# Performance work log

Hardware: AMD Instinct MI355X
Metric: run time of the kernel (lower is better)

## Reference

```python
import jax, jax.numpy as jnp
import numpy as np

NUM_CLASSES = 10
HIDDEN = 64
_LABEL2MASK_THRESHOL = 500


def setup_inputs() -> dict:
    key = jax.random.key(0)
    ks = jax.random.split(key, 8)
    B, h, w = 4, 60, 80
    feature1 = jax.random.normal(ks[0], (B, 512, h, w), dtype=jnp.float32)
    feature2 = jax.random.normal(ks[1], (B, 512, h // 2, w // 2), dtype=jnp.float32)
    # kaiming fan_in init for 1x1 convs: std = sqrt(2/fan_in)
    w1 = jax.random.normal(ks[2], (HIDDEN, 512), dtype=jnp.float32) * np.sqrt(2.0 / 512)
    b1 = jnp.zeros((HIDDEN,), dtype=jnp.float32)
    w2 = jax.random.normal(ks[3], (HIDDEN, 512), dtype=jnp.float32) * np.sqrt(2.0 / 512)
    b2 = jnp.zeros((HIDDEN,), dtype=jnp.float32)
    wo = jax.random.normal(ks[4], (NUM_CLASSES + 1, HIDDEN), dtype=jnp.float32) * np.sqrt(2.0 / HIDDEN)
    bo = jnp.zeros((NUM_CLASSES + 1,), dtype=jnp.float32)
    return {"feature1": feature1, "feature2": feature2, "w1": w1, "b1": b1,
            "w2": w2, "b2": b2, "wo": wo, "bo": bo}


def conv1x1(x, w, b):
    # x: (B,C,H,W), w: (O,C) -> (B,O,H,W)
    return jnp.einsum('bchw,oc->bohw', x, w) + b[None, :, None, None]


def label2bbx(seg, num_classes):
    # seg: (B,H,W) int labels. Vectorized per-(batch,class) min/max reduction
    # replacing the original python double loop. Fixed output shape
    # (B*(num_classes-1), 6); rows failing the pixel-count threshold are -1.
    B, H, W = seg.shape
    classes = jnp.arange(1, num_classes)  # cls_id != 0, covers 1..num_classes-1
    mask = seg[:, None, :, :] == classes[None, :, None, None]  # (B,C-1,H,W)
    count = mask.sum(axis=(2, 3))
    xs = jnp.arange(W)
    ys = jnp.arange(H)
    big = jnp.int32(2 ** 30)
    xmin = jnp.where(mask, xs[None, None, None, :], big).min(axis=(2, 3))
    xmax = jnp.where(mask, xs[None, None, None, :], -1).max(axis=(2, 3))
    ymin = jnp.where(mask, ys[None, None, :, None], big).min(axis=(2, 3))
    ymax = jnp.where(mask, ys[None, None, :, None], -1).max(axis=(2, 3))
    valid = count >= _LABEL2MASK_THRESHOL
    batch_ids = jnp.broadcast_to(jnp.arange(B)[:, None], (B, num_classes - 1))
    cls_ids = jnp.broadcast_to(classes[None, :], (B, num_classes - 1))
    rows = jnp.stack([batch_ids, xmin, ymin, xmax, ymax, cls_ids], axis=-1)
    rows = jnp.where(valid[..., None], rows, -1)
    return rows.reshape(-1, 6)


def reference(feature1, feature2, w1, b1, w2, b2, wo, bo):
    feat1 = jax.nn.relu(conv1x1(feature1, w1, b1))          # (B,64,h,w)
    feat2 = jax.nn.relu(conv1x1(feature2, w2, b2))          # (B,64,h/2,w/2)
    feat2_up = jnp.repeat(jnp.repeat(feat2, 2, axis=2), 2, axis=3)
    combo = feat1 + feat2_up
    # nearest upsample scale_factor=8
    combo_up = jnp.repeat(jnp.repeat(combo, 8, axis=2), 8, axis=3)  # (B,64,8h,8w)
    out = jax.nn.relu(conv1x1(combo_up, wo, bo))            # (B,11,8h,8w)
    probability = jax.nn.softmax(out, axis=1)
    segmentation = jnp.argmax(probability, axis=1)
    bbx = label2bbx(segmentation, NUM_CLASSES)
    return probability, segmentation, bbx
```

## Files before the change

kernel.cpp:

```cpp
#include <hip/hip_runtime.h>
#include <math.h>

#define NB   4
#define CIN  512
#define HID  64
#define NK   11
#define H1   60
#define W1p  80
#define P1   4800
#define H2   30
#define W2p  40
#define P2   1200
#define HO   480
#define WOp  640
#define NP1  (NB*P1)
#define NP2  (NB*P2)
#define PLANE ((size_t)HO*WOp)
#define SEG_OFF ((size_t)NB*NK*PLANE)
#define BBX_OFF (SEG_OFF + (size_t)NB*PLANE)

#define WS_WT1 0
#define WS_WT2 32768
#define WS_C1  65536
#define WS_F2  (WS_C1 + NP1*64)
#define WS_PRB (WS_F2 + NP2*64)
#define WS_SEG (WS_PRB + NP1*12)

__global__ __launch_bounds__(256) void transpose_w(const float* __restrict__ w1,
                                                   const float* __restrict__ w2,
                                                   float* __restrict__ ws) {
    int i = blockIdx.x * 256 + threadIdx.x;
    if (i >= HID * CIN) return;
    int o = i >> 9;
    int c = i & 511;
    ws[WS_WT1 + c * HID + o] = w1[i];
    ws[WS_WT2 + c * HID + o] = w2[i];
}

__global__ __launch_bounds__(256) void conv_krg(const float* __restrict__ f1,
                                                const float* __restrict__ f2,
                                                const float* __restrict__ wt1,
                                                const float* __restrict__ wt2,
                                                const float* __restrict__ b1v,
                                                const float* __restrict__ b2v,
                                                float* __restrict__ c1o,
                                                float* __restrict__ f2o) {
    __shared__ float red[3][16][256];
    int D = blockIdx.x;
    int L = (D & 7) * 48 + (D >> 3);
    int tile = L >> 2;
    int rg   = L & 3;
    const float* X; const float* wT; const float* bias; float* Cout;
    int P, px0;
    if (tile < 76) {
        int b = tile / 19; int ti = tile % 19;
        px0 = ti * 256; if (px0 > P1 - 256) px0 = P1 - 256;
        X = f1 + (size_t)b * CIN * P1;  P = P1;  wT = wt1;  bias = b1v;
        Cout = c1o + (size_t)b * P1 * 64;
    } else {
        int u = tile - 76; int b = u / 5; int ti = u % 5;
        px0 = ti * 256; if (px0 > P2 - 256) px0 = P2 - 256;
        X = f2 + (size_t)b * CIN * P2;  P = P2;  wT = wt2;  bias = b2v;
        Cout = f2o + (size_t)b * P2 * 64;
    }
    int lane  = threadIdx.x & 63;
    int kq    = threadIdx.x >> 6;
    int cbase = __builtin_amdgcn_readfirstlane(kq << 7);
    int row0  = rg << 4;

    const float* Xp = X + (size_t)cbase * P + px0 + lane * 4;
    const float* Wp = wT + (size_t)cbase * 64 + row0;

    float acc[16][4];
#pragma unroll
    for (int r = 0; r < 16; ++r)
#pragma unroll
        for (int q = 0; q < 4; ++q) acc[r][q] = 0.f;

    float4 xa[4], xn[4];
#pragma unroll
    for (int i = 0; i < 4; ++i) xa[i] = *(const float4*)(Xp + (size_t)i * P);

    for (int c0 = 0; c0 < 128; c0 += 4) {
        if (c0 < 124) {
#pragma unroll
            for (int i = 0; i < 4; ++i)
                xn[i] = *(const float4*)(Xp + (size_t)(c0 + 4 + i) * P);
        }
#pragma unroll
        for (int i = 0; i < 4; ++i) {
            const float* wr = Wp + (size_t)(c0 + i) * 64;
            float4 x = xa[i];
#pragma unroll
            for (int r4 = 0; r4 < 4; ++r4) {
                float4 w = *(const float4*)(wr + r4 * 4);
#pragma unroll
                for (int j = 0; j < 4; ++j) {
                    int r = r4 * 4 + j;
                    float wv = (j == 0) ? w.x : (j == 1) ? w.y : (j == 2) ? w.z : w.w;
                    acc[r][0] = fmaf(x.x, wv, acc[r][0]);
                    acc[r][1] = fmaf(x.y, wv, acc[r][1]);
                    acc[r][2] = fmaf(x.z, wv, acc[r][2]);
                    acc[r][3] = fmaf(x.w, wv, acc[r][3]);
                }
            }
        }
#pragma unroll
        for (int i = 0; i < 4; ++i) xa[i] = xn[i];
    }

    if (kq > 0) {
#pragma unroll
        for (int r = 0; r < 16; ++r)
            *(float4*)&red[kq - 1][r][lane * 4] =
                make_float4(acc[r][0], acc[r][1], acc[r][2], acc[r][3]);
    }
    __syncthreads();
    if (kq == 0) {
        float v[16][4];
#pragma unroll
        for (int r = 0; r < 16; ++r) {
            float4 s0 = *(float4*)&red[0][r][lane * 4];
            float4 s1 = *(float4*)&red[1][r][lane * 4];
            float4 s2 = *(float4*)&red[2][r][lane * 4];
            float bb = bias[row0 + r];
            float a0 = acc[r][0] + s0.x + s1.x + s2.x + bb;
            float a1 = acc[r][1] + s0.y + s1.y + s2.y + bb;
            float a2 = acc[r][2] + s0.z + s1.z + s2.z + bb;
            float a3 = acc[r][3] + s0.w + s1.w + s2.w + bb;
            v[r][0] = a0 > 0.f ? a0 : 0.f;
            v[r][1] = a1 > 0.f ? a1 : 0.f;
            v[r][2] = a2 > 0.f ? a2 : 0.f;
            v[r][3] = a3 > 0.f ? a3 : 0.f;
        }
#pragma unroll
        for (int q = 0; q < 4; ++q) {
            float* op = Cout + (size_t)(px0 + lane * 4 + q) * 64 + row0;
#pragma unroll
            for (int r4 = 0; r4 < 4; ++r4)
                *(float4*)(op + r4 * 4) = make_float4(v[r4*4+0][q], v[r4*4+1][q],
                                                      v[r4*4+2][q], v[r4*4+3][q]);
        }
    }
}

__global__ __launch_bounds__(256) void head_kernel(const float* __restrict__ wo,
                                                   const float* __restrict__ bo,
                                                   float* __restrict__ ws) {
    __shared__ float swo[NK * 64];
    __shared__ float sbo[NK];
    for (int i = threadIdx.x; i < NK * 64; i += 256) swo[i] = wo[i];
    if (threadIdx.x < NK) sbo[threadIdx.x] = bo[threadIdx.x];
    __syncthreads();

    int p  = blockIdx.x * 256 + threadIdx.x;
    int b  = p / P1;
    int pb = p % P1;
    int y  = pb / W1p, x = pb % W1p;
    int qp = (y >> 1) * W2p + (x >> 1);
    const float* c1p = ws + WS_C1 + ((size_t)b * P1 + pb) * 64;
    const float* f2p = ws + WS_F2 + ((size_t)b * P2 + qp) * 64;

    float ok[NK];
#pragma unroll
    for (int k = 0; k < NK; ++k) ok[k] = sbo[k];
#pragma unroll
    for (int o4 = 0; o4 < 16; ++o4) {
        float4 c1q = *(const float4*)(c1p + o4 * 4);
        float4 f2q = *(const float4*)(f2p + o4 * 4);
        float co[4] = { c1q.x + f2q.x, c1q.y + f2q.y, c1q.z + f2q.z, c1q.w + f2q.w };
#pragma unroll
        for (int j = 0; j < 4; ++j) {
            int o = o4 * 4 + j;
#pragma unroll
            for (int k = 0; k < NK; ++k) ok[k] = fmaf(co[j], swo[k * 64 + o], ok[k]);
        }
    }
    float m = 0.f;
#pragma unroll
    for (int k = 0; k < NK; ++k) {
        ok[k] = ok[k] > 0.f ? ok[k] : 0.f;
        if (ok[k] > m) m = ok[k];
    }
    float e[NK], sum = 0.f;
#pragma unroll
    for (int k = 0; k < NK; ++k) { e[k] = expf(ok[k] - m); sum += e[k]; }
    float inv = 1.f / sum;
    int arg = 0; float best = ok[0];
#pragma unroll
    for (int k = 1; k < NK; ++k) { if (ok[k] > best) { best = ok[k]; arg = k; } }

    float* pr = ws + WS_PRB + (size_t)p * 12;
#pragma unroll
    for (int k = 0; k < NK; ++k) pr[k] = e[k] * inv;
    pr[11] = (float)arg;
    ((int*)(ws + WS_SEG))[p] = arg;
}

__global__ __launch_bounds__(256) void upsample_kernel(const float* __restrict__ ws,
                                                       float* __restrict__ out) {
    const float* prb = ws + WS_PRB;
    unsigned total4 = (unsigned)((SEG_OFF + (size_t)NB * PLANE) / 4);
    unsigned step = gridDim.x * 256;
    for (unsigned i4 = blockIdx.x * 256 + threadIdx.x; i4 < total4; i4 += step) {
        unsigned f = i4 * 4;
        float v;
        if (f < (unsigned)SEG_OFF) {
            unsigned plane = f / (unsigned)PLANE;
            unsigned r = f - plane * (unsigned)PLANE;
            unsigned b = plane / NK, k = plane - b * NK;
            unsigned y = r / WOp, x = r - y * WOp;
            unsigned p = b * P1 + (y >> 3) * W1p + (x >> 3);
            v = prb[p * 12 + k];
        } else {
            unsigned g = f - (unsigned)SEG_OFF;
            unsigned b = g / (unsigned)PLANE;
            unsigned r = g - b * (unsigned)PLANE;
            unsigned y = r / WOp, x = r - y * WOp;
            unsigned p = b * P1 + (y >> 3) * W1p + (x >> 3);
            v = prb[p * 12 + 11];
        }
        *(float4*)(out + f) = make_float4(v, v, v, v);
    }
}

__global__ __launch_bounds__(256) void bbx_kernel(const float* __restrict__ ws,
                                                  float* __restrict__ out) {
    __shared__ int cnt[10], xmn[10], xmx[10], ymn[10], ymx[10];
    int b = blockIdx.x;
    int t = threadIdx.x;
    if (t < 10) { cnt[t] = 0; xmn[t] = 1 << 30; xmx[t] = -1; ymn[t] = 1 << 30; ymx[t] = -1; }
    __syncthreads();
    const int* seg = (const int*)(ws + WS_SEG) + b * P1;
    for (int p = t; p < P1; p += 256) {
        int s = seg[p];
        if (s >= 1 && s <= 9) {
            int y = p / W1p, x = p % W1p;
            atomicAdd(&cnt[s], 1);
            atomicMin(&xmn[s], x); atomicMax(&xmx[s], x);
            atomicMin(&ymn[s], y); atomicMax(&ymx[s], y);
        }
    }
    __syncthreads();
    if (t < 9) {
        int c = t + 1;
        bool valid = cnt[c] * 64 >= 500;
        float r[6];
        if (valid) {
            r[0] = (float)b;
            r[1] = (float)(xmn[c] * 8);
            r[2] = (float)(ymn[c] * 8);
            r[3] = (float)(xmx[c] * 8 + 7);
            r[4] = (float)(ymx[c] * 8 + 7);
            r[5] = (float)c;
        } else {
            for (int i = 0; i < 6; ++i) r[i] = -1.f;
        }
        float* row = out + BBX_OFF + (size_t)(b * 9 + t) * 6;
        for (int i = 0; i < 6; ++i) row[i] = r[i];
    }
}

extern "C" void kernel_launch(void* const* d_in, const int* in_sizes, int n_in,
                              void* d_out, int out_size, void* d_ws, size_t ws_size,
                              hipStream_t stream) {
    const float* f1 = (const float*)d_in[0];
    const float* f2 = (const float*)d_in[1];
    const float* w1 = (const float*)d_in[2];
    const float* b1 = (const float*)d_in[3];
    const float* w2 = (const float*)d_in[4];
    const float* b2 = (const float*)d_in[5];
    const float* wo = (const float*)d_in[6];
    const float* bo = (const float*)d_in[7];
    float* ws  = (float*)d_ws;
    float* out = (float*)d_out;

    transpose_w<<<128, 256, 0, stream>>>(w1, w2, ws);
    conv_krg<<<384, 256, 0, stream>>>(f1, f2, ws + WS_WT1, ws + WS_WT2,
                                      b1, b2, ws + WS_C1, ws + WS_F2);
    head_kernel<<<75, 256, 0, stream>>>(wo, bo, ws);
    upsample_kernel<<<2048, 256, 0, stream>>>(ws, out);
    bbx_kernel<<<NB, 256, 0, stream>>>(ws, out);
}
```

Measured before the change: 68.34 us.

## Split conv output rows into 8-row groups, stage weights in LDS, deepen prefetch

The 1x1 conv kernel now gives each block 8 output channels instead of 16, which doubles the grid to 768 blocks. Each block stages its weight slice (512x8) in shared memory rather than reading the weights from global memory. Input loads are double-buffered in chunks of 8 channels to hide latency better. The trade is that each input tile is now read from global memory by twice as many blocks, and there is an extra sync and LDS fill per block. In return the kernel gets more parallelism and lower register pressure.

```diff
diff --git a/kernel.cpp b/kernel.cpp
--- a/kernel.cpp
+++ b/kernel.cpp
@@ -37,7 +37,7 @@
     ws[WS_WT2 + c * HID + o] = w2[i];
 }
 
-__global__ __launch_bounds__(256) void conv_krg(const float* __restrict__ f1,
+__global__ __launch_bounds__(256) void conv_v10(const float* __restrict__ f1,
                                                 const float* __restrict__ f2,
                                                 const float* __restrict__ wt1,
                                                 const float* __restrict__ wt2,
@@ -45,11 +45,14 @@
                                                 const float* __restrict__ b2v,
                                                 float* __restrict__ c1o,
                                                 float* __restrict__ f2o) {
-    __shared__ float red[3][16][256];
+    __shared__ float wlds[CIN * 8];
+    __shared__ float red[3][8][256];
     int D = blockIdx.x;
-    int L = (D & 7) * 48 + (D >> 3);
-    int tile = L >> 2;
-    int rg   = L & 3;
+    int L = (D & 7) * 96 + (D >> 3);
+    int tile = L >> 3;
+    int rg   = L & 7;
+    int row0 = rg << 3;
+
     const float* X; const float* wT; const float* bias; float* Cout;
     int P, px0;
     if (tile < 76) {
@@ -63,63 +66,84 @@
         X = f2 + (size_t)b * CIN * P2;  P = P2;  wT = wt2;  bias = b2v;
         Cout = f2o + (size_t)b * P2 * 64;
     }
+
+    {
+        int t = threadIdx.x;
+        int c2 = t >> 1, part = (t & 1) * 4;
+#pragma unroll
+        for (int i = 0; i < 4; ++i) {
+            int c = c2 + i * 128;
+            float4 w = *(const float4*)(wT + (size_t)c * 64 + row0 + part);
+            *(float4*)&wlds[c * 8 + part] = w;
+        }
+    }
+    __syncthreads();
+
     int lane  = threadIdx.x & 63;
     int kq    = threadIdx.x >> 6;
-    int cbase = __builtin_amdgcn_readfirstlane(kq << 7);
-    int row0  = rg << 4;
+    int cbase = kq << 7;
 
     const float* Xp = X + (size_t)cbase * P + px0 + lane * 4;
-    const float* Wp = wT + (size_t)cbase * 64 + row0;
-
-    float acc[16][4];
-#pragma unroll
-    for (int r = 0; r < 16; ++r)
+
+    float acc[8][4];
+#pragma unroll
+    for (int r = 0; r < 8; ++r)
 #pragma unroll
         for (int q = 0; q < 4; ++q) acc[r][q] = 0.f;
 
-    float4 xa[4], xn[4];
-#pragma unroll
-    for (int i = 0; i < 4; ++i) xa[i] = *(const float4*)(Xp + (size_t)i * P);
-
-    for (int c0 = 0; c0 < 128; c0 += 4) {
-        if (c0 < 124) {
-#pragma unroll
-            for (int i = 0; i < 4; ++i)
-                xn[i] = *(const float4*)(Xp + (size_t)(c0 + 4 + i) * P);
-        }
-#pragma unroll
-        for (int i = 0; i < 4; ++i) {
-            const float* wr = Wp + (size_t)(c0 + i) * 64;
-            float4 x = xa[i];
-#pragma unroll
-            for (int r4 = 0; r4 < 4; ++r4) {
-                float4 w = *(const float4*)(wr + r4 * 4);
-#pragma unroll
-                for (int j = 0; j < 4; ++j) {
-                    int r = r4 * 4 + j;
-                    float wv = (j == 0) ? w.x : (j == 1) ? w.y : (j == 2) ? w.z : w.w;
-                    acc[r][0] = fmaf(x.x, wv, acc[r][0]);
-                    acc[r][1] = fmaf(x.y, wv, acc[r][1]);
-                    acc[r][2] = fmaf(x.z, wv, acc[r][2]);
-                    acc[r][3] = fmaf(x.w, wv, acc[r][3]);
-                }
+    float4 xA[8], xB[8];
+
+    auto comp8 = [&](const float4* xb, int cq) {
+#pragma unroll
+        for (int i = 0; i < 8; ++i) {
+            const float* wq = wlds + (size_t)(cbase + cq + i) * 8;
+            float4 w0 = *(const float4*)(wq);
+            float4 w1 = *(const float4*)(wq + 4);
+            float4 x  = xb[i];
+#pragma unroll
+            for (int j = 0; j < 4; ++j) {
+                float wv0 = (j == 0) ? w0.x : (j == 1) ? w0.y : (j == 2) ? w0.z : w0.w;
+                float wv1 = (j == 0) ? w1.x : (j == 1) ? w1.y : (j == 2) ? w1.z : w1.w;
+                acc[j][0]     = fmaf(x.x, wv0, acc[j][0]);
+                acc[j][1]     = fmaf(x.y, wv0, acc[j][1]);
+                acc[j][2]     = fmaf(x.z, wv0, acc[j][2]);
+                acc[j][3]     = fmaf(x.w, wv0, acc[j][3]);
+                acc[j + 4][0] = fmaf(x.x, wv1, acc[j + 4][0]);
+                acc[j + 4][1] = fmaf(x.y, wv1, acc[j + 4][1]);
+                acc[j + 4][2] = fmaf(x.z, wv1, acc[j + 4][2]);
+                acc[j + 4][3] = fmaf(x.w, wv1, acc[j + 4][3]);
             }
         }
-#pragma unroll
-        for (int i = 0; i < 4; ++i) xa[i] = xn[i];
+    };
+
+#pragma unroll
+    for (int i = 0; i < 8; ++i) xA[i] = *(const float4*)(Xp + (size_t)i * P);
+
+    for (int it = 0; it < 8; ++it) {
+        int c0 = it * 16;
+#pragma unroll
+        for (int i = 0; i < 8; ++i)
+            xB[i] = *(const float4*)(Xp + (size_t)(c0 + 8 + i) * P);
+        comp8(xA, c0);
+        if (it < 7) {
+#pragma unroll
+            for (int i = 0; i < 8; ++i)
+                xA[i] = *(const float4*)(Xp + (size_t)(c0 + 16 + i) * P);
+        }
+        comp8(xB, c0 + 8);
     }
 
     if (kq > 0) {
 #pragma unroll
-        for (int r = 0; r < 16; ++r)
+        for (int r = 0; r < 8; ++r)
             *(float4*)&red[kq - 1][r][lane * 4] =
                 make_float4(acc[r][0], acc[r][1], acc[r][2], acc[r][3]);
     }
     __syncthreads();
     if (kq == 0) {
-        float v[16][4];
-#pragma unroll
-        for (int r = 0; r < 16; ++r) {
+        float v[8][4];
+#pragma unroll
+        for (int r = 0; r < 8; ++r) {
             float4 s0 = *(float4*)&red[0][r][lane * 4];
             float4 s1 = *(float4*)&red[1][r][lane * 4];
             float4 s2 = *(float4*)&red[2][r][lane * 4];
@@ -136,10 +160,8 @@
 #pragma unroll
         for (int q = 0; q < 4; ++q) {
             float* op = Cout + (size_t)(px0 + lane * 4 + q) * 64 + row0;
-#pragma unroll
-            for (int r4 = 0; r4 < 4; ++r4)
-                *(float4*)(op + r4 * 4) = make_float4(v[r4*4+0][q], v[r4*4+1][q],
-                                                      v[r4*4+2][q], v[r4*4+3][q]);
+            *(float4*)(op)     = make_float4(v[0][q], v[1][q], v[2][q], v[3][q]);
+            *(float4*)(op + 4) = make_float4(v[4][q], v[5][q], v[6][q], v[7][q]);
         }
     }
 }
@@ -276,7 +298,7 @@
     float* out = (float*)d_out;
 
     transpose_w<<<128, 256, 0, stream>>>(w1, w2, ws);
-    conv_krg<<<384, 256, 0, stream>>>(f1, f2, ws + WS_WT1, ws + WS_WT2,
+    conv_v10<<<768, 256, 0, stream>>>(f1, f2, ws + WS_WT1, ws + WS_WT2,
                                       b1, b2, ws + WS_C1, ws + WS_F2);
     head_kernel<<<75, 256, 0, stream>>>(wo, bo, ws);
     upsample_kernel<<<2048, 256, 0, stream>>>(ws, out);
```

After: 65.89 us. 1.04x faster.
